# Kernel optimization log

Hardware: AMD Instinct MI355X
Metric: run time of the kernel (lower is better)

Reference implementation:

```python
import jax, jax.numpy as jnp
import numpy as np

VOCAB = 100000
EMB = 256
HID = 512
H2 = HID // 2
TAGS = 6
START = 3
STOP = 4
NEG = -10000.0
T = 4096


def setup_inputs() -> dict:
    key = jax.random.key(0)
    ks = jax.random.split(key, 16)
    s = 0.05
    trans = jax.random.normal(ks[12], (TAGS, TAGS), dtype=jnp.float32)
    trans = trans.at[START, :].set(NEG).at[:, STOP].set(NEG)
    return {
        "sentence": jax.random.randint(ks[0], (T,), 0, VOCAB, dtype=jnp.int32),
        "emb": jax.random.normal(ks[1], (VOCAB, EMB), dtype=jnp.float32) * s,
        "w_ih_f": jax.random.normal(ks[2], (4 * H2, EMB), dtype=jnp.float32) * s,
        "w_hh_f": jax.random.normal(ks[3], (4 * H2, H2), dtype=jnp.float32) * s,
        "b_ih_f": jax.random.normal(ks[4], (4 * H2,), dtype=jnp.float32) * s,
        "b_hh_f": jax.random.normal(ks[5], (4 * H2,), dtype=jnp.float32) * s,
        "w_ih_b": jax.random.normal(ks[6], (4 * H2, EMB), dtype=jnp.float32) * s,
        "w_hh_b": jax.random.normal(ks[7], (4 * H2, H2), dtype=jnp.float32) * s,
        "b_ih_b": jax.random.normal(ks[8], (4 * H2,), dtype=jnp.float32) * s,
        "b_hh_b": jax.random.normal(ks[9], (4 * H2,), dtype=jnp.float32) * s,
        "W_out": jax.random.normal(ks[10], (TAGS, HID), dtype=jnp.float32) * s,
        "b_out": jax.random.normal(ks[11], (TAGS,), dtype=jnp.float32) * s,
        "transitions": trans,
        "h0": jax.random.normal(ks[13], (2, H2), dtype=jnp.float32),
        "c0": jax.random.normal(ks[14], (2, H2), dtype=jnp.float32),
    }


def _lstm_dir(x, h0, c0, w_ih, w_hh, b_ih, b_hh, reverse):
    # x: (T, E); PyTorch LSTM gate order i, f, g, o
    def step(carry, xt):
        h, c = carry
        z = xt @ w_ih.T + b_ih + h @ w_hh.T + b_hh
        i, f, g, o = jnp.split(z, 4)
        i = jax.nn.sigmoid(i)
        f = jax.nn.sigmoid(f)
        g = jnp.tanh(g)
        o = jax.nn.sigmoid(o)
        c = f * c + i * g
        h = o * jnp.tanh(c)
        return (h, c), h

    _, hs = jax.lax.scan(step, (h0, c0), x, reverse=reverse)
    return hs  # (T, H2), time-aligned for both directions


def reference(sentence, emb, w_ih_f, w_hh_f, b_ih_f, b_hh_f,
              w_ih_b, w_hh_b, b_ih_b, b_hh_b, W_out, b_out,
              transitions, h0, c0):
    x = emb[sentence]  # (T, E)
    hf = _lstm_dir(x, h0[0], c0[0], w_ih_f, w_hh_f, b_ih_f, b_hh_f, False)
    hb = _lstm_dir(x, h0[1], c0[1], w_ih_b, w_hh_b, b_ih_b, b_hh_b, True)
    feats = jnp.concatenate([hf, hb], axis=-1) @ W_out.T + b_out  # (T, TAGS)

    init = jnp.full((TAGS,), NEG, dtype=feats.dtype).at[START].set(0.0)

    def vstep(fv, feat):
        tmp = transitions + fv[None, :]          # (to, from)
        bp = jnp.argmax(tmp, axis=1)             # best prev tag per next tag
        fv_new = tmp[jnp.arange(TAGS), bp] + feat
        return fv_new, bp

    fv, bptrs = jax.lax.scan(vstep, init, feats)  # bptrs: (T, TAGS)
    term = fv + transitions[STOP]
    best = jnp.argmax(term)
    score = term[best]

    def btstep(tag, bp):
        return bp[tag], tag

    _, path = jax.lax.scan(btstep, best, bptrs, reverse=True)  # (T,)
    return score, path
```

## Files before the change

kernel.cpp:

```cpp
#include <hip/hip_runtime.h>
#include <stdint.h>
#include <math.h>

#define T 4096
#define NTAGS 6
#define START_TAG 3
#define STOP_TAG 4
#define NEGV -10000.0f

__device__ __forceinline__ float sigm_fast(float z) {
  return 1.f / (1.f + __expf(-z));
}
__device__ __forceinline__ float tanh_fast(float z) {
  return 1.f - 2.f / (1.f + __expf(2.f * z));
}

typedef _Float16 half2v __attribute__((ext_vector_type(2)));
__device__ __forceinline__ float dot2acc(unsigned a, unsigned b, float c) {
  return __builtin_amdgcn_fdot2(__builtin_bit_cast(half2v, a),
                                __builtin_bit_cast(half2v, b), c, false);
}
__device__ __forceinline__ unsigned short f16b(float x) {
  _Float16 h = (_Float16)x;
  return __builtin_bit_cast(unsigned short, h);
}

__global__ __launch_bounds__(256) void k0_prep(
    const float* __restrict__ wf, const float* __restrict__ wb,
    const float* __restrict__ bif, const float* __restrict__ bhf,
    const float* __restrict__ bib, const float* __restrict__ bhb,
    float* __restrict__ wT, float* __restrict__ bias2) {
  int idx = blockIdx.x * 256 + threadIdx.x;
  int k = idx >> 11, col = idx & 2047;
  int d = col >> 10, g = col & 1023;
  const float* w = d ? wb : wf;
  wT[idx] = w[g * 256 + k];
  if (idx < 2048) bias2[idx] = d ? (bib[g] + bhb[g]) : (bif[g] + bhf[g]);
}

__global__ __launch_bounds__(256) void k1_zpre(
    const int* __restrict__ sent, const float* __restrict__ emb,
    const float* __restrict__ wT, const float* __restrict__ bias2,
    float* __restrict__ zpre) {
  int tb = blockIdx.x, cb = blockIdx.y;
  int tid = threadIdx.x;
  int col = cb * 256 + tid;
  int d = col >> 10, g = col & 1023;
  __shared__ float xs[32 * 256];
  int t0 = tb * 32;
  for (int r = 0; r < 32; r++) {
    int s = sent[t0 + r];
    xs[r * 256 + tid] = emb[(size_t)s * 256 + tid];
  }
  __syncthreads();
  float acc[32];
#pragma unroll
  for (int r = 0; r < 32; r++) acc[r] = 0.f;
  const float4* xs4 = (const float4*)xs;
  for (int kq = 0; kq < 64; kq++) {
    float w0 = wT[(4 * kq + 0) * 2048 + col];
    float w1 = wT[(4 * kq + 1) * 2048 + col];
    float w2 = wT[(4 * kq + 2) * 2048 + col];
    float w3 = wT[(4 * kq + 3) * 2048 + col];
#pragma unroll
    for (int r = 0; r < 32; r++) {
      float4 x4 = xs4[r * 64 + kq];
      acc[r] += w0 * x4.x + w1 * x4.y + w2 * x4.z + w3 * x4.w;
    }
  }
  float bb = bias2[col];
  for (int r = 0; r < 32; r++)
    zpre[((size_t)d * T + (t0 + r)) * 1024 + g] = acc[r] + bb;
}

__global__ __launch_bounds__(256) void k2_lstm(
    const float* __restrict__ zpre,
    const float* __restrict__ whf, const float* __restrict__ whb,
    const float* __restrict__ h0, const float* __restrict__ c0,
    float* h_all, unsigned long long* ring) {
  int w = blockIdx.x;
  int d = w >> 4, sub = w & 15;
  const float* w_hh = d ? whb : whf;
  int tid = threadIdx.x;
  int q = tid >> 6, lane = tid & 63;

  __shared__ uint4 wl4[32 * 64];
  __shared__ __align__(16) unsigned hq[4][32];
  __shared__ float z_part[4][64];

  {
    unsigned short* wlh = (unsigned short*)wl4;
    for (int idx = tid; idx < 64 * 256; idx += 256) {
      int r = idx >> 8, k = idx & 255;
      int gate = r >> 4, cell = r & 15;
      float wv = w_hh[(size_t)(gate * 256 + sub * 16 + cell) * 256 + k];
      int sq = k >> 6, sm = (k >> 3) & 7, sj = k & 7;
      wlh[((sq * 8 + sm) * 64 + r) * 8 + sj] = f16b(wv);
    }
  }
  if (lane < 32) {
    float f0 = h0[d * 256 + q * 64 + 2 * lane];
    float f1 = h0[d * 256 + q * 64 + 2 * lane + 1];
    hq[q][lane] = (unsigned)f16b(f0) | ((unsigned)f16b(f1) << 16);
  }
  float c = 0.f;
  if (tid < 16) c = c0[d * 256 + sub * 16 + tid];

  const float* zp_d = zpre + (size_t)d * T * 1024;
  float* h_d = h_all + (size_t)d * T * 256;
  unsigned long long* rg = ring + (size_t)d * 2 * 128;

  float zv4[4] = {0.f, 0.f, 0.f, 0.f};
  if (tid < 16) {
    int t0 = d ? (T - 1) : 0;
#pragma unroll
    for (int g = 0; g < 4; g++)
      zv4[g] = zp_d[(size_t)t0 * 1024 + g * 256 + sub * 16 + tid];
  }
  __syncthreads();

  for (int s = 0; s < T; s++) {
    int t = d ? (T - 1 - s) : s;
    float zn4[4] = {0.f, 0.f, 0.f, 0.f};
    if (tid < 16 && s + 1 < T) {
      int tn = d ? (t - 1) : (t + 1);
#pragma unroll
      for (int g = 0; g < 4; g++)
        zn4[g] = zp_d[(size_t)tn * 1024 + g * 256 + sub * 16 + tid];
    }

    if (s > 0 && lane < 32) {
      unsigned exp_tag = (unsigned)s;
      unsigned long long* addr = &rg[((s - 1) & 1) * 128 + q * 32 + lane];
      unsigned long long v;
      do {
        v = __hip_atomic_load(addr, __ATOMIC_RELAXED, __HIP_MEMORY_SCOPE_AGENT);
      } while ((unsigned)(v >> 32) != exp_tag);
      hq[q][lane] = (unsigned)v;
    }
    __builtin_amdgcn_wave_barrier();

    const uint4* hv = (const uint4*)hq[q];
    float acc = 0.f;
#pragma unroll
    for (int m = 0; m < 8; m++) {
      uint4 wv4 = wl4[(q * 8 + m) * 64 + lane];
      uint4 hv4 = hv[m];
      acc = dot2acc(wv4.x, hv4.x, acc);
      acc = dot2acc(wv4.y, hv4.y, acc);
      acc = dot2acc(wv4.z, hv4.z, acc);
      acc = dot2acc(wv4.w, hv4.w, acc);
    }
    z_part[q][lane] = acc;
    __syncthreads();

    if (tid < 16) {
      float a[4];
#pragma unroll
      for (int g = 0; g < 4; g++) {
        int r = g * 16 + tid;
        float z = z_part[0][r] + z_part[1][r] + z_part[2][r] + z_part[3][r]
                + zv4[g];
        a[g] = (g == 2) ? tanh_fast(z) : sigm_fast(z);
      }
      c = a[1] * c + a[0] * a[2];
      float hvl = a[3] * tanh_fast(c);
      h_d[(size_t)t * 256 + sub * 16 + tid] = hvl;
      float hn = __shfl_down(hvl, 1);
      if ((tid & 1) == 0) {
        unsigned h2 = (unsigned)f16b(hvl) | ((unsigned)f16b(hn) << 16);
        __hip_atomic_store(&rg[(s & 1) * 128 + sub * 8 + (tid >> 1)],
                           ((unsigned long long)(unsigned)(s + 1) << 32) | h2,
                           __ATOMIC_RELAXED, __HIP_MEMORY_SCOPE_AGENT);
      }
#pragma unroll
      for (int g = 0; g < 4; g++) zv4[g] = zn4[g];
    }
    __syncthreads();
  }
}

__global__ __launch_bounds__(64) void k3_feats(
    const float* __restrict__ h_all, const float* __restrict__ Wout,
    const float* __restrict__ bout, float* __restrict__ feats) {
  int t = blockIdx.x;
  int j = threadIdx.x;
  const float* hf = h_all + (size_t)t * 256;
  const float* hb = h_all + (size_t)T * 256 + (size_t)t * 256;
  float s[6];
#pragma unroll
  for (int g = 0; g < 6; g++) s[g] = 0.f;
#pragma unroll
  for (int m = 0; m < 4; m++) {
    float a = hf[j + 64 * m];
#pragma unroll
    for (int g = 0; g < 6; g++) s[g] += a * Wout[g * 512 + j + 64 * m];
  }
#pragma unroll
  for (int m = 0; m < 4; m++) {
    float b = hb[j + 64 * m];
#pragma unroll
    for (int g = 0; g < 6; g++) s[g] += b * Wout[g * 512 + 256 + j + 64 * m];
  }
#pragma unroll
  for (int g = 0; g < 6; g++) {
#pragma unroll
    for (int off = 32; off >= 1; off >>= 1) s[g] += __shfl_xor(s[g], off);
  }
  if (j < 6) feats[(size_t)t * 6 + j] = s[j] + bout[j];
}

__global__ __launch_bounds__(64) void k4_viterbi(
    const float* __restrict__ feats, const float* __restrict__ trans,
    float* __restrict__ out) {
  __shared__ unsigned char bp_lds[T * 8];
  __shared__ float fbuf[2][64 * 6];
  int lane = threadIdx.x;

  float tr[6];
#pragma unroll
  for (int f = 0; f < 6; f++) tr[f] = (lane < 6) ? trans[lane * 6 + f] : 0.f;
  float fv = (lane == START_TAG) ? 0.f : NEGV;

  for (int idx = lane; idx < 384; idx += 64) fbuf[0][idx] = feats[idx];

  for (int cch = 0; cch < 64; cch++) {
    float pf[6];
    if (cch + 1 < 64) {
#pragma unroll
      for (int m = 0; m < 6; m++)
        pf[m] = feats[(cch + 1) * 384 + lane + 64 * m];
    }
    const float* fb = fbuf[cch & 1];
    for (int j = 0; j < 64; j++) {
      int t = cch * 64 + j;
      float best = -3.4e38f;
      int bi = 0;
#pragma unroll
      for (int f = 0; f < 6; f++) {
        float v = __shfl(fv, f) + tr[f];
        if (v > best) { best = v; bi = f; }
      }
      float nfv = best + fb[j * 6 + (lane < 6 ? lane : 0)];
      if (lane < 6) {
        fv = nfv;
        bp_lds[t * 8 + lane] = (unsigned char)bi;
      }
    }
    if (cch + 1 < 64) {
#pragma unroll
      for (int m = 0; m < 6; m++)
        fbuf[(cch + 1) & 1][lane + 64 * m] = pf[m];
    }
  }

  float term = (lane < 6) ? (fv + trans[STOP_TAG * 6 + lane]) : -3.4e38f;
  float bestv = -3.4e38f;
  int bestt = 0;
#pragma unroll
  for (int f = 0; f < 6; f++) {
    float v = __shfl(term, f);
    if (v > bestv) { bestv = v; bestt = f; }
  }
  if (lane == 0) out[0] = bestv;

  unsigned int ident = 0;
#pragma unroll
  for (int i = 0; i < 6; i++) ident |= (unsigned)i << (3 * i);

  unsigned int p = ident;
  int base = lane * 64;
  for (int j2 = 0; j2 < 64; j2++) {
    const unsigned int* bw = (const unsigned int*)&bp_lds[(base + j2) * 8];
    unsigned int lo = bw[0], hi = bw[1];
    unsigned int mw = (lo & 7) | (((lo >> 8) & 7) << 3) | (((lo >> 16) & 7) << 6)
                    | (((lo >> 24) & 7) << 9) | ((hi & 7) << 12)
                    | (((hi >> 8) & 7) << 15);
    unsigned int np = 0;
#pragma unroll
    for (int i = 0; i < 6; i++) {
      unsigned int b = (mw >> (3 * i)) & 7;
      np |= ((p >> (3 * b)) & 7) << (3 * i);
    }
    p = np;
  }
  unsigned int suf = p;
#pragma unroll
  for (int off = 1; off < 64; off <<= 1) {
    unsigned int other = __shfl_down(suf, off);
    if (lane + off < 64) {
      unsigned int ns = 0;
#pragma unroll
      for (int i = 0; i < 6; i++) {
        unsigned int b = (other >> (3 * i)) & 7;
        ns |= ((suf >> (3 * b)) & 7) << (3 * i);
      }
      suf = ns;
    }
  }
  unsigned int tail = __shfl_down(suf, 1);
  if (lane == 63) tail = ident;
  unsigned int cur = tail;
  for (int j2 = 63; j2 >= 0; j2--) {
    int t = base + j2;
    out[1 + t] = (float)((cur >> (3 * bestt)) & 7);
    const unsigned int* bw = (const unsigned int*)&bp_lds[t * 8];
    unsigned int lo = bw[0], hi = bw[1];
    unsigned int mw = (lo & 7) | (((lo >> 8) & 7) << 3) | (((lo >> 16) & 7) << 6)
                    | (((lo >> 24) & 7) << 9) | ((hi & 7) << 12)
                    | (((hi >> 8) & 7) << 15);
    unsigned int nc = 0;
#pragma unroll
    for (int i = 0; i < 6; i++) {
      unsigned int b = (cur >> (3 * i)) & 7;
      nc |= ((mw >> (3 * b)) & 7) << (3 * i);
    }
    cur = nc;
  }
}

extern "C" void kernel_launch(void* const* d_in, const int* in_sizes, int n_in,
                              void* d_out, int out_size, void* d_ws, size_t ws_size,
                              hipStream_t stream) {
  const int*   sent  = (const int*)d_in[0];
  const float* emb   = (const float*)d_in[1];
  const float* wihf  = (const float*)d_in[2];
  const float* whhf  = (const float*)d_in[3];
  const float* bihf  = (const float*)d_in[4];
  const float* bhhf  = (const float*)d_in[5];
  const float* wihb  = (const float*)d_in[6];
  const float* whhb  = (const float*)d_in[7];
  const float* bihb  = (const float*)d_in[8];
  const float* bhhb  = (const float*)d_in[9];
  const float* Wout  = (const float*)d_in[10];
  const float* bout  = (const float*)d_in[11];
  const float* trans = (const float*)d_in[12];
  const float* h0    = (const float*)d_in[13];
  const float* c0    = (const float*)d_in[14];
  float* out = (float*)d_out;

  char* ws = (char*)d_ws;
  float*              zpre  = (float*)(ws + 0);
  float*              h_all = (float*)(ws + 33554432);
  float*              wT    = (float*)(ws + 41943040);
  float*              bias2 = (float*)(ws + 44040192);
  float*              feats = (float*)(ws + 44048384);
  unsigned long long* ring  = (unsigned long long*)(ws + 44146688);

  k0_prep<<<2048, 256, 0, stream>>>(wihf, wihb, bihf, bhhf, bihb, bhhb, wT, bias2);
  dim3 g1(128, 8);
  k1_zpre<<<g1, 256, 0, stream>>>(sent, emb, wT, bias2, zpre);
  k2_lstm<<<32, 256, 0, stream>>>(zpre, whhf, whhb, h0, c0, h_all, ring);
  k3_feats<<<4096, 64, 0, stream>>>(h_all, Wout, bout, feats);
  k4_viterbi<<<1, 64, 0, stream>>>(feats, trans, out);
}
```

Before: 6.460 ms.

## Restructure LSTM recurrence to per-wave register weights with shuffle reductions, no block barriers

The recurrent kernel now keeps each thread's fp16 W_hh slice in registers instead of LDS. Each wave fully owns 4 cells, so the gate reduction and nonlinearity run through cross-lane shuffles, and the two __syncthreads per timestep go away. The pre-activation layout is reordered so the four gates of a cell are contiguous, letting each lane load one z value. This shortens the serial per-step critical path. In exchange every wave polls the ring independently and register pressure goes up.

After: 9.513 ms. 47.3% more time.

```diff
diff --git a/kernel.cpp b/kernel.cpp
--- a/kernel.cpp
+++ b/kernel.cpp
@@ -32,10 +32,13 @@
     float* __restrict__ wT, float* __restrict__ bias2) {
   int idx = blockIdx.x * 256 + threadIdx.x;
   int k = idx >> 11, col = idx & 2047;
-  int d = col >> 10, g = col & 1023;
+  int d = col >> 10, low = col & 1023;
+  int cc = low >> 2, g = low & 3;
+  int grow = g * 256 + cc;
   const float* w = d ? wb : wf;
-  wT[idx] = w[g * 256 + k];
-  if (idx < 2048) bias2[idx] = d ? (bib[g] + bhb[g]) : (bif[g] + bhf[g]);
+  wT[idx] = w[grow * 256 + k];
+  if (idx < 2048)
+    bias2[idx] = d ? (bib[grow] + bhb[grow]) : (bif[grow] + bhf[grow]);
 }
 
 __global__ __launch_bounds__(256) void k1_zpre(
@@ -45,7 +48,7 @@
   int tb = blockIdx.x, cb = blockIdx.y;
   int tid = threadIdx.x;
   int col = cb * 256 + tid;
-  int d = col >> 10, g = col & 1023;
+  int d = col >> 10, low = col & 1023;
   __shared__ float xs[32 * 256];
   int t0 = tb * 32;
   for (int r = 0; r < 32; r++) {
@@ -70,7 +73,7 @@
   }
   float bb = bias2[col];
   for (int r = 0; r < 32; r++)
-    zpre[((size_t)d * T + (t0 + r)) * 1024 + g] = acc[r] + bb;
+    zpre[((size_t)d * T + (t0 + r)) * 1024 + low] = acc[r] + bb;
 }
 
 __global__ __launch_bounds__(256) void k2_lstm(
@@ -82,101 +85,96 @@
   int d = w >> 4, sub = w & 15;
   const float* w_hh = d ? whb : whf;
   int tid = threadIdx.x;
-  int q = tid >> 6, lane = tid & 63;
-
-  __shared__ uint4 wl4[32 * 64];
-  __shared__ __align__(16) unsigned hq[4][32];
-  __shared__ float z_part[4][64];
-
+  int q = tid >> 6, l = tid & 63;
+  int j = l >> 4, g = (l >> 2) & 3, s = l & 3;
+  int cell = sub * 16 + q * 4 + j;
+  int row = g * 256 + cell;
+
+  __shared__ __align__(16) unsigned hq[4][4][36];
+
+  unsigned wreg[32];
   {
-    unsigned short* wlh = (unsigned short*)wl4;
-    for (int idx = tid; idx < 64 * 256; idx += 256) {
-      int r = idx >> 8, k = idx & 255;
-      int gate = r >> 4, cell = r & 15;
-      float wv = w_hh[(size_t)(gate * 256 + sub * 16 + cell) * 256 + k];
-      int sq = k >> 6, sm = (k >> 3) & 7, sj = k & 7;
-      wlh[((sq * 8 + sm) * 64 + r) * 8 + sj] = f16b(wv);
-    }
-  }
-  if (lane < 32) {
-    float f0 = h0[d * 256 + q * 64 + 2 * lane];
-    float f1 = h0[d * 256 + q * 64 + 2 * lane + 1];
-    hq[q][lane] = (unsigned)f16b(f0) | ((unsigned)f16b(f1) << 16);
-  }
-  float c = 0.f;
-  if (tid < 16) c = c0[d * 256 + sub * 16 + tid];
-
+    const float4* wp = (const float4*)(w_hh + (size_t)row * 256 + s * 64);
+#pragma unroll
+    for (int m = 0; m < 16; m++) {
+      float4 v = wp[m];
+      wreg[2 * m]     = (unsigned)f16b(v.x) | ((unsigned)f16b(v.y) << 16);
+      wreg[2 * m + 1] = (unsigned)f16b(v.z) | ((unsigned)f16b(v.w) << 16);
+    }
+  }
+  {
+    float4 h4 = *(const float4*)(h0 + d * 256 + 4 * l);
+    unsigned e0 = (unsigned)f16b(h4.x) | ((unsigned)f16b(h4.y) << 16);
+    unsigned e1 = (unsigned)f16b(h4.z) | ((unsigned)f16b(h4.w) << 16);
+    *(unsigned long long*)&hq[q][l >> 4][(2 * l) & 31] =
+        ((unsigned long long)e1 << 32) | e0;
+  }
+
+  float c = c0[d * 256 + cell];
   const float* zp_d = zpre + (size_t)d * T * 1024;
   float* h_d = h_all + (size_t)d * T * 256;
   unsigned long long* rg = ring + (size_t)d * 2 * 128;
-
-  float zv4[4] = {0.f, 0.f, 0.f, 0.f};
-  if (tid < 16) {
-    int t0 = d ? (T - 1) : 0;
-#pragma unroll
-    for (int g = 0; g < 4; g++)
-      zv4[g] = zp_d[(size_t)t0 * 1024 + g * 256 + sub * 16 + tid];
-  }
-  __syncthreads();
-
-  for (int s = 0; s < T; s++) {
-    int t = d ? (T - 1 - s) : s;
-    float zn4[4] = {0.f, 0.f, 0.f, 0.f};
-    if (tid < 16 && s + 1 < T) {
+  int zoff = sub * 64 + (q * 4 + j) * 4 + g;
+
+  int t0 = d ? (T - 1) : 0;
+  float zv = zp_d[(size_t)t0 * 1024 + zoff];
+
+  for (int st = 0; st < T; st++) {
+    int t = d ? (T - 1 - st) : st;
+    float zn = 0.f;
+    if (st + 1 < T) {
       int tn = d ? (t - 1) : (t + 1);
-#pragma unroll
-      for (int g = 0; g < 4; g++)
-        zn4[g] = zp_d[(size_t)tn * 1024 + g * 256 + sub * 16 + tid];
-    }
-
-    if (s > 0 && lane < 32) {
-      unsigned exp_tag = (unsigned)s;
-      unsigned long long* addr = &rg[((s - 1) & 1) * 128 + q * 32 + lane];
-      unsigned long long v;
-      do {
-        v = __hip_atomic_load(addr, __ATOMIC_RELAXED, __HIP_MEMORY_SCOPE_AGENT);
-      } while ((unsigned)(v >> 32) != exp_tag);
-      hq[q][lane] = (unsigned)v;
+      zn = zp_d[(size_t)tn * 1024 + zoff];
+    }
+    if (st > 0) {
+      unsigned exp_tag = (unsigned)st;
+      unsigned long long* a0 = &rg[((st - 1) & 1) * 128 + 2 * l];
+      unsigned long long v0 =
+          __hip_atomic_load(a0, __ATOMIC_RELAXED, __HIP_MEMORY_SCOPE_AGENT);
+      unsigned long long v1 =
+          __hip_atomic_load(a0 + 1, __ATOMIC_RELAXED, __HIP_MEMORY_SCOPE_AGENT);
+      while ((unsigned)(v0 >> 32) != exp_tag)
+        v0 = __hip_atomic_load(a0, __ATOMIC_RELAXED, __HIP_MEMORY_SCOPE_AGENT);
+      while ((unsigned)(v1 >> 32) != exp_tag)
+        v1 = __hip_atomic_load(a0 + 1, __ATOMIC_RELAXED,
+                               __HIP_MEMORY_SCOPE_AGENT);
+      *(unsigned long long*)&hq[q][l >> 4][(2 * l) & 31] =
+          (v1 << 32) | (unsigned)v0;
     }
     __builtin_amdgcn_wave_barrier();
 
-    const uint4* hv = (const uint4*)hq[q];
+    const uint4* hp = (const uint4*)&hq[q][s][0];
     float acc = 0.f;
 #pragma unroll
     for (int m = 0; m < 8; m++) {
-      uint4 wv4 = wl4[(q * 8 + m) * 64 + lane];
-      uint4 hv4 = hv[m];
-      acc = dot2acc(wv4.x, hv4.x, acc);
-      acc = dot2acc(wv4.y, hv4.y, acc);
-      acc = dot2acc(wv4.z, hv4.z, acc);
-      acc = dot2acc(wv4.w, hv4.w, acc);
-    }
-    z_part[q][lane] = acc;
-    __syncthreads();
-
-    if (tid < 16) {
-      float a[4];
-#pragma unroll
-      for (int g = 0; g < 4; g++) {
-        int r = g * 16 + tid;
-        float z = z_part[0][r] + z_part[1][r] + z_part[2][r] + z_part[3][r]
-                + zv4[g];
-        a[g] = (g == 2) ? tanh_fast(z) : sigm_fast(z);
-      }
-      c = a[1] * c + a[0] * a[2];
-      float hvl = a[3] * tanh_fast(c);
-      h_d[(size_t)t * 256 + sub * 16 + tid] = hvl;
-      float hn = __shfl_down(hvl, 1);
-      if ((tid & 1) == 0) {
-        unsigned h2 = (unsigned)f16b(hvl) | ((unsigned)f16b(hn) << 16);
-        __hip_atomic_store(&rg[(s & 1) * 128 + sub * 8 + (tid >> 1)],
-                           ((unsigned long long)(unsigned)(s + 1) << 32) | h2,
-                           __ATOMIC_RELAXED, __HIP_MEMORY_SCOPE_AGENT);
-      }
-#pragma unroll
-      for (int g = 0; g < 4; g++) zv4[g] = zn4[g];
-    }
-    __syncthreads();
+      uint4 h4 = hp[m];
+      acc = dot2acc(wreg[4 * m + 0], h4.x, acc);
+      acc = dot2acc(wreg[4 * m + 1], h4.y, acc);
+      acc = dot2acc(wreg[4 * m + 2], h4.z, acc);
+      acc = dot2acc(wreg[4 * m + 3], h4.w, acc);
+    }
+    acc += __shfl_xor(acc, 1);
+    acc += __shfl_xor(acc, 2);
+    float z = acc + zv;
+    float a = (g == 2) ? tanh_fast(z) : sigm_fast(z);
+    int base = l & 0x33;
+    float ai = __shfl(a, base);
+    float af = __shfl(a, base | 4);
+    float ag = __shfl(a, base | 8);
+    float ao = __shfl(a, base | 12);
+    c = af * c + ai * ag;
+    float hvl = ao * tanh_fast(c);
+    float hnx = __shfl(hvl, l + 16);
+
+    if ((l & 15) == 0)
+      h_d[(size_t)t * 256 + cell] = hvl;
+    if ((l & 31) == 0) {
+      unsigned h2 = (unsigned)f16b(hvl) | ((unsigned)f16b(hnx) << 16);
+      __hip_atomic_store(&rg[(st & 1) * 128 + sub * 8 + q * 2 + (j >> 1)],
+                         ((unsigned long long)(unsigned)(st + 1) << 32) | h2,
+                         __ATOMIC_RELAXED, __HIP_MEMORY_SCOPE_AGENT);
+    }
+    zv = zn;
   }
 }
 
```
